# Optimization experiments

Hardware: AMD Instinct MI355X
Metric: run time of the kernel (lower is better)

## Reference

```python
import jax, jax.numpy as jnp
import numpy as np

N_HEADS = 8
EMBED_C = 256  # key/query channels
OUT_C = 256    # value/output channels
MASK_CENTER = True

def setup_inputs() -> dict:
    key = jax.random.key(0)
    ks = jax.random.split(key, 5)
    B, C, H, W = 32, 256, 32, 32
    x = jax.random.normal(ks[0], (B, C, H, W), dtype=jnp.float32)
    # 1x1 conv weights as [out, in] matrices; scaled like torch conv default init
    s = 1.0 / np.sqrt(C)
    q_w = jax.random.normal(ks[1], (EMBED_C, C), dtype=jnp.float32) * s
    q_b = jax.random.normal(ks[2], (EMBED_C,), dtype=jnp.float32) * s
    kv_w = jax.random.normal(ks[3], (EMBED_C + OUT_C, C), dtype=jnp.float32) * s
    kv_b = jax.random.normal(ks[4], (EMBED_C + OUT_C,), dtype=jnp.float32) * s
    return {"x": x, "q_w": q_w, "q_b": q_b, "kv_w": kv_w, "kv_b": kv_b}

def _to_multihead(t):
    # t: (B, C, S) -> (B, n_heads, S, C // n_heads)
    B, C, S = t.shape
    return jnp.transpose(t.reshape(B, N_HEADS, C // N_HEADS, S), (0, 1, 3, 2))

def reference(x, q_w, q_b, kv_w, kv_b):
    B, C, H, W = x.shape
    S = H * W
    xf = x.reshape(B, C, S)  # flatten spatial; 1x1 conv == channel matmul
    q = jnp.einsum('oc,bcs->bos', q_w, xf) + q_b[None, :, None]
    kv = jnp.einsum('oc,bcs->bos', kv_w, xf) + kv_b[None, :, None]
    k, v = kv[:, :EMBED_C], kv[:, EMBED_C:]
    q = _to_multihead(q)   # (B, h, S, dk)
    k = _to_multihead(k)   # (B, h, S, dk)
    v = _to_multihead(v)   # (B, h, S, dv)
    dk = k.shape[-1]
    # strictly-lower-triangular causal mask (center pixel masked)
    mask = jnp.tril(jnp.ones((S, S), dtype=x.dtype), -int(MASK_CENTER))
    scores = jnp.einsum('bhqd,bhkd->bhqk', q, k) / jnp.sqrt(jnp.asarray(dk, x.dtype))
    scores = jnp.where(mask == 0, jnp.asarray(-10000.0, x.dtype), scores)
    attn = jax.nn.softmax(scores, axis=-1)
    attn = jnp.where(mask == 0, jnp.asarray(0.0, x.dtype), attn)
    out = jnp.einsum('bhqk,bhkd->bhqd', attn, v)  # (B, h, S, dv)
    out = jnp.transpose(out, (0, 1, 3, 2)).reshape(B, OUT_C, H, W)
    return out
```

## Files before the change

kernel.cpp:

```cpp
#include <hip/hip_runtime.h>
#include <hip/hip_bf16.h>

typedef __attribute__((ext_vector_type(8))) short short8;
typedef __attribute__((ext_vector_type(4))) float f32x4;
typedef __attribute__((ext_vector_type(16))) float f32x16;

#define B_  32
#define CH  256
#define S_  1024
#define NH  8
#define HD  32

static __device__ __forceinline__ unsigned short f2bf(float f) {
  __hip_bfloat16 h = __float2bfloat16(f);
  return *reinterpret_cast<unsigned short*>(&h);
}

static __device__ __forceinline__ void gl_lds16(const void* g, void* l) {
  __builtin_amdgcn_global_load_lds(
      (const __attribute__((address_space(1))) void*)g,
      (__attribute__((address_space(3))) void*)l, 16, 0, 0);
}

__global__ void k_prep(const float* __restrict__ x, unsigned short* __restrict__ xt,
                       const float* __restrict__ qw, const float* __restrict__ qb,
                       const float* __restrict__ kvw, const float* __restrict__ kvb,
                       unsigned short* __restrict__ wt, float* __restrict__ bias) {
  __shared__ float tile[32][33];
  int blk = (int)blockIdx.x;
  int t = threadIdx.x;
  if (blk < 8192) {
    int b = blk >> 8;
    int inner = blk & 255;
    int ct = inner >> 5, st = inner & 31;
    int c0 = ct * 32, s0 = st * 32;
    int r = t >> 3, q4 = (t & 7) * 4;
    const float4 v = *reinterpret_cast<const float4*>(
        x + ((size_t)(b * CH + c0 + r)) * S_ + s0 + q4);
    tile[r][q4 + 0] = v.x; tile[r][q4 + 1] = v.y;
    tile[r][q4 + 2] = v.z; tile[r][q4 + 3] = v.w;
    __syncthreads();
    ushort4 u;
    u.x = f2bf(tile[q4 + 0][r]); u.y = f2bf(tile[q4 + 1][r]);
    u.z = f2bf(tile[q4 + 2][r]); u.w = f2bf(tile[q4 + 3][r]);
    *reinterpret_cast<ushort4*>(xt + ((size_t)(b * S_ + s0 + r)) * CH + c0 + q4) = u;
  } else {
    int gid = (blk - 8192) * 256 + t;
    const float rs = 0.25503531838951954f;
    int o = gid >> 8, c = gid & 255;
    float v = (o < 256) ? qw[o * 256 + c] * rs : kvw[(o - 256) * 256 + c];
    wt[gid] = f2bf(v);
    if (gid < 768) bias[gid] = (gid < 256) ? qb[gid] * rs : kvb[gid - 256];
  }
}

__global__ __launch_bounds__(256, 6) void k_proj(
    const unsigned short* __restrict__ wt, const float* __restrict__ bias,
    const unsigned short* __restrict__ xt,
    unsigned short* __restrict__ qws, unsigned short* __restrict__ kv) {
  __shared__ __align__(16) union {
    struct { unsigned short As[2][2048]; unsigned short Bs[2][2048]; } g;
    unsigned short vst[8192];
  } SH;
  int b = blockIdx.y;
  int mt = blockIdx.x >> 4, nt = blockIdx.x & 15;
  int tid = threadIdx.x;
  int wid = tid >> 6, l = tid & 63;
  int rb = l >> 4, lr = l & 15;
  int wr = wid >> 1, wc = wid & 1;
  int mb = mt * 64, nb = nt * 64;
  int wm = wr * 32, wn = wc * 32;
  const unsigned short* xb = xt + (size_t)b * S_ * CH;

  int r0 = tid >> 2, k0 = (tid & 3) * 8;
  const unsigned short* wa0 = wt + (size_t)(mb + r0) * CH + k0;
  const unsigned short* xb0 = xb + (size_t)(nb + r0) * CH + k0;
  char* asb = (char*)&SH.g.As[0][0];
  char* bsb = (char*)&SH.g.Bs[0][0];
  int wb = wid * 1024;

  f32x4 acc[2][2];
  #pragma unroll
  for (int mf = 0; mf < 2; ++mf)
    #pragma unroll
    for (int nf = 0; nf < 2; ++nf)
      acc[mf][nf] = (f32x4){0.f, 0.f, 0.f, 0.f};

  gl_lds16(wa0, asb + wb);
  gl_lds16(xb0, bsb + wb);
  __syncthreads();

  #pragma unroll 1
  for (int kk = 0; kk < 8; ++kk) {
    int cur = kk & 1;
    if (kk < 7) {
      int ko = (kk + 1) * 32;
      gl_lds16(wa0 + ko, asb + (cur ^ 1) * 4096 + wb);
      gl_lds16(xb0 + ko, bsb + (cur ^ 1) * 4096 + wb);
    }

    short8 a[2], bfr[2];
    #pragma unroll
    for (int mf = 0; mf < 2; ++mf)
      a[mf] = *reinterpret_cast<const short8*>(
          &SH.g.As[cur][(wm + mf * 16 + lr) * 32 + rb * 8]);
    #pragma unroll
    for (int nf = 0; nf < 2; ++nf)
      bfr[nf] = *reinterpret_cast<const short8*>(
          &SH.g.Bs[cur][(wn + nf * 16 + lr) * 32 + rb * 8]);
    #pragma unroll
    for (int mf = 0; mf < 2; ++mf)
      #pragma unroll
      for (int nf = 0; nf < 2; ++nf)
        acc[mf][nf] = __builtin_amdgcn_mfma_f32_16x16x32_bf16(
            a[mf], bfr[nf], acc[mf][nf], 0, 0, 0);

    __syncthreads();
  }

  if (mb < 256) {
    #pragma unroll
    for (int mf = 0; mf < 2; ++mf) {
      int m0 = mb + wm + mf * 16 + rb * 4;
      const float4 bv = *reinterpret_cast<const float4*>(bias + m0);
      #pragma unroll
      for (int nf = 0; nf < 2; ++nf) {
        int n = nb + wn + nf * 16 + lr;
        ushort4 u = {f2bf(acc[mf][nf][0] + bv.x), f2bf(acc[mf][nf][1] + bv.y),
                     f2bf(acc[mf][nf][2] + bv.z), f2bf(acc[mf][nf][3] + bv.w)};
        int h = m0 >> 5, d = m0 & 31;
        *reinterpret_cast<ushort4*>(
            qws + ((size_t)(b * NH + h) * S_ + n) * HD + d) = u;
      }
    }
  } else {
    const bool isV = (mb >= 512);
    const int voff = isV ? 1024 : 0;
    unsigned short* vst = SH.vst;
    #pragma unroll
    for (int mf = 0; mf < 2; ++mf) {
      int m0 = mb + wm + mf * 16 + rb * 4;
      const float4 bv = *reinterpret_cast<const float4*>(bias + m0);
      int mml = wm + mf * 16 + rb * 4;
      int hl = mml >> 5, d0 = mml & 31;
      #pragma unroll
      for (int nf = 0; nf < 2; ++nf) {
        int nlc = wn + nf * 16 + lr;
        int tl = nlc >> 5, nl = nlc & 31;
        float v0 = acc[mf][nf][0] + bv.x;
        float v1 = acc[mf][nf][1] + bv.y;
        float v2 = acc[mf][nf][2] + bv.z;
        float v3 = acc[mf][nf][3] + bv.w;
        int tb = (hl * 2 + tl) * 1024;
        if (isV) {
          int kp = (nl & 19) | (((nl >> 2) & 1) << 3) | (((nl >> 3) & 1) << 2);
          int base = tb + (kp >> 3) * 256 + (kp & 7);
          vst[base + (size_t)(d0 + 0) * 8] = f2bf(v0);
          vst[base + (size_t)(d0 + 1) * 8] = f2bf(v1);
          vst[base + (size_t)(d0 + 2) * 8] = f2bf(v2);
          vst[base + (size_t)(d0 + 3) * 8] = f2bf(v3);
        } else {
          ushort4 u = {f2bf(v0), f2bf(v1), f2bf(v2), f2bf(v3)};
          *reinterpret_cast<ushort4*>(
              &vst[tb + (d0 >> 3) * 256 + nl * 8 + (d0 & 7)]) = u;
        }
      }
    }
    __syncthreads();
    int tt = tid >> 6, j = tid & 63;
    int hb = (isV ? (mb - 512) : (mb - 256)) >> 5;
    int h = hb + (tt >> 1);
    size_t gb = ((size_t)(b * NH + h) * 32 + (nt * 2 + (tt & 1))) * 2048 + voff;
    #pragma unroll
    for (int s = 0; s < 2; ++s) {
      int off = (j + s * 64) * 8;
      *reinterpret_cast<short8*>(kv + gb + off) =
          *reinterpret_cast<const short8*>(vst + tt * 1024 + off);
    }
  }
}

__global__ __launch_bounds__(512, 4) void k_attn(
    const unsigned short* __restrict__ qws, const unsigned short* __restrict__ kv,
    float* __restrict__ out) {
  __shared__ __align__(16) unsigned short kvbuf[2][8192];
  int tid = threadIdx.x;
  int wid = tid >> 6, l = tid & 63;
  int col = l & 31, hi = l >> 5;
  int bh = (int)(blockIdx.x & 255);
  int g  = 3 - (int)(blockIdx.x >> 8);
  int qt = g * 8 + wid;
  int q0 = qt << 5;
  int niter = g * 2 + 2;

  const unsigned short* Q   = qws + (size_t)bh * S_ * HD;
  const unsigned short* kvb = kv + (size_t)bh * 32 * 2048;
  char* kb0 = (char*)&kvbuf[0][0];
  int wb = wid * 1024;

  short8 aq0 = *reinterpret_cast<const short8*>(Q + (q0 + col) * HD + hi * 8);
  short8 aq1 = *reinterpret_cast<const short8*>(Q + (q0 + col) * HD + 16 + hi * 8);

  f32x16 z, O;
  #pragma unroll
  for (int i = 0; i < 16; ++i) { z[i] = 0.f; O[i] = 0.f; }
  float lsA = 0.f, lsB = 0.f;

  gl_lds16(kvb + tid * 8,        kb0 + wb);
  gl_lds16(kvb + 4096 + tid * 8, kb0 + 8192 + wb);
  __syncthreads();

  #pragma unroll 1
  for (int i = 0; i < niter; ++i) {
    int cur = i & 1;
    bool more = (i + 1 < niter);
    if (more) {
      const unsigned short* src = kvb + (size_t)(i + 1) * 8192 + tid * 8;
      char* dst = kb0 + (cur ^ 1) * 16384 + wb;
      gl_lds16(src,        dst);
      gl_lds16(src + 4096, dst + 8192);
    }

    #pragma unroll
    for (int sub = 0; sub < 4; ++sub) {
      int t = 4 * i + sub;
      if (qt >= t) {
        const unsigned short* Kb = &kvbuf[cur][sub * 2048];
        short8 bk0 = *reinterpret_cast<const short8*>(Kb + hi * 256 + col * 8);
        short8 bk1 = *reinterpret_cast<const short8*>(Kb + 512 + hi * 256 + col * 8);
        short8 av0 = *reinterpret_cast<const short8*>(Kb + 1024 + hi * 256 + col * 8);
        short8 av1 = *reinterpret_cast<const short8*>(Kb + 1536 + hi * 256 + col * 8);

        f32x16 st = __builtin_amdgcn_mfma_f32_32x32x16_bf16(bk0, aq0, z, 0, 0, 0);
        st = __builtin_amdgcn_mfma_f32_32x32x16_bf16(bk1, aq1, st, 0, 0, 0);

        float p[16];
        if (t == qt) {
          #pragma unroll
          for (int r = 0; r < 16; ++r) {
            int key = (r & 3) + 8 * (r >> 2) + 4 * hi;
            float e = __builtin_amdgcn_exp2f(st[r]);
            p[r] = (key < col) ? e : 0.f;
          }
        } else {
          #pragma unroll
          for (int r = 0; r < 16; ++r) p[r] = __builtin_amdgcn_exp2f(st[r]);
        }

        lsA += ((p[0] + p[1]) + (p[2] + p[3])) + ((p[4] + p[5]) + (p[6] + p[7]));
        lsB += ((p[8] + p[9]) + (p[10] + p[11])) + ((p[12] + p[13]) + (p[14] + p[15]));

        union { unsigned int u[8]; short8 v[2]; } pb;
        #pragma unroll
        for (int jj = 0; jj < 8; ++jj)
          asm("v_cvt_pk_bf16_f32 %0, %1, %2"
              : "=v"(pb.u[jj]) : "v"(p[2 * jj]), "v"(p[2 * jj + 1]));

        O = __builtin_amdgcn_mfma_f32_32x32x16_bf16(av0, pb.v[0], O, 0, 0, 0);
        O = __builtin_amdgcn_mfma_f32_32x32x16_bf16(av1, pb.v[1], O, 0, 0, 0);
      }
    }

    __syncthreads();
  }

  float lsum = lsA + lsB;
  float ltot = lsum + __shfl_xor(lsum, 32);
  float linv = (ltot > 0.f) ? 1.f / ltot : 0.f;
  int b = bh >> 3, h = bh & 7;
  float* ob = out + ((size_t)(b * 256 + h * 32)) * S_ + q0 + col;
  #pragma unroll
  for (int r = 0; r < 16; ++r) {
    int d = (r & 3) + 8 * (r >> 2) + 4 * hi;
    ob[(size_t)d * S_] = O[r] * linv;
  }
}

extern "C" void kernel_launch(void* const* d_in, const int* in_sizes, int n_in,
                              void* d_out, int out_size, void* d_ws, size_t ws_size,
                              hipStream_t stream) {
  const float* x   = (const float*)d_in[0];
  const float* qw  = (const float*)d_in[1];
  const float* qb  = (const float*)d_in[2];
  const float* kvw = (const float*)d_in[3];
  const float* kvb = (const float*)d_in[4];
  float* out = (float*)d_out;

  char* ws = (char*)d_ws;
  unsigned short* wt   = (unsigned short*)(ws + 0);
  float*          bias = (float*)(ws + 393216);
  unsigned short* xt   = (unsigned short*)(ws + 396288);
  unsigned short* qws  = (unsigned short*)(ws + 17173504);
  unsigned short* kv   = (unsigned short*)(ws + 33950720);

  k_prep<<<8960, 256, 0, stream>>>(x, xt, qw, qb, kvw, kvb, wt, bias);
  k_proj<<<dim3(192, 32), 256, 0, stream>>>(wt, bias, xt, qws, kv);
  k_attn<<<1024, 512, 0, stream>>>(qws, kv, out);
}
```

Before: 77.79 us.

## Keep X tile resident in LDS and loop projection over all output rows

The projection kernel now loads each 64-column slice of the transposed input into LDS once (full K=256) and has a 512-thread block loop over all 768 output channels in 128-row chunks. Weight fragments are read directly from global memory into registers with a small software prefetch, instead of being staged through double-buffered LDS. This removes re-reading the same X tile for each of the 12 output-row tiles and drops per-k-step barriers. The trade-off is a much smaller grid (512 blocks), serialized output-row work per block, and uncached global weight loads on the MFMA critical path.

Result: no change. 76.87 us (-1.2%).

```diff
diff --git a/kernel.cpp b/kernel.cpp
--- a/kernel.cpp
+++ b/kernel.cpp
@@ -54,128 +54,118 @@
   }
 }
 
-__global__ __launch_bounds__(256, 6) void k_proj(
+__global__ __launch_bounds__(512) void k_proj(
     const unsigned short* __restrict__ wt, const float* __restrict__ bias,
     const unsigned short* __restrict__ xt,
     unsigned short* __restrict__ qws, unsigned short* __restrict__ kv) {
-  __shared__ __align__(16) union {
-    struct { unsigned short As[2][2048]; unsigned short Bs[2][2048]; } g;
-    unsigned short vst[8192];
-  } SH;
-  int b = blockIdx.y;
-  int mt = blockIdx.x >> 4, nt = blockIdx.x & 15;
+  __shared__ __align__(16) unsigned short Bs[16384];
+  __shared__ __align__(16) unsigned short vst[8192];
+  int b = (int)blockIdx.x >> 4, nt = (int)blockIdx.x & 15;
   int tid = threadIdx.x;
   int wid = tid >> 6, l = tid & 63;
   int rb = l >> 4, lr = l & 15;
-  int wr = wid >> 1, wc = wid & 1;
-  int mb = mt * 64, nb = nt * 64;
-  int wm = wr * 32, wn = wc * 32;
+  int nb = nt * 64;
   const unsigned short* xb = xt + (size_t)b * S_ * CH;
 
-  int r0 = tid >> 2, k0 = (tid & 3) * 8;
-  const unsigned short* wa0 = wt + (size_t)(mb + r0) * CH + k0;
-  const unsigned short* xb0 = xb + (size_t)(nb + r0) * CH + k0;
-  char* asb = (char*)&SH.g.As[0][0];
-  char* bsb = (char*)&SH.g.Bs[0][0];
-  int wb = wid * 1024;
-
-  f32x4 acc[2][2];
-  #pragma unroll
-  for (int mf = 0; mf < 2; ++mf)
+  {
+    int row = (tid & 255) >> 2, kkh = tid >> 8, ch = tid & 3;
+    const unsigned short* bsrc = xb + (size_t)(nb + row) * CH + kkh * 32 + ch * 8;
+    char* bsb = (char*)Bs;
+    int wb = wid * 1024;
     #pragma unroll
-    for (int nf = 0; nf < 2; ++nf)
-      acc[mf][nf] = (f32x4){0.f, 0.f, 0.f, 0.f};
-
-  gl_lds16(wa0, asb + wb);
-  gl_lds16(xb0, bsb + wb);
+    for (int q = 0; q < 4; ++q)
+      gl_lds16(bsrc + q * 64, bsb + q * 8192 + wb);
+  }
   __syncthreads();
 
   #pragma unroll 1
-  for (int kk = 0; kk < 8; ++kk) {
-    int cur = kk & 1;
-    if (kk < 7) {
-      int ko = (kk + 1) * 32;
-      gl_lds16(wa0 + ko, asb + (cur ^ 1) * 4096 + wb);
-      gl_lds16(xb0 + ko, bsb + (cur ^ 1) * 4096 + wb);
-    }
-
-    short8 a[2], bfr[2];
+  for (int mt = 0; mt < 6; ++mt) {
+    int mb = mt * 128;
+    const unsigned short* wA = wt + (size_t)(mb + wid * 16 + lr) * CH + rb * 8;
+
+    f32x4 acc[4];
     #pragma unroll
-    for (int mf = 0; mf < 2; ++mf)
-      a[mf] = *reinterpret_cast<const short8*>(
-          &SH.g.As[cur][(wm + mf * 16 + lr) * 32 + rb * 8]);
-    #pragma unroll
-    for (int nf = 0; nf < 2; ++nf)
-      bfr[nf] = *reinterpret_cast<const short8*>(
-          &SH.g.Bs[cur][(wn + nf * 16 + lr) * 32 + rb * 8]);
-    #pragma unroll
-    for (int mf = 0; mf < 2; ++mf)
+    for (int nf = 0; nf < 4; ++nf) acc[nf] = (f32x4){0.f, 0.f, 0.f, 0.f};
+
+#define CMPA(A8, kk) do {                                           \
+    _Pragma("unroll")                                               \
+    for (int nf = 0; nf < 4; ++nf) {                                \
+      short8 bfr = *reinterpret_cast<const short8*>(                \
+          &Bs[(kk) * 2048 + (nf * 16 + lr) * 32 + rb * 8]);         \
+      acc[nf] = __builtin_amdgcn_mfma_f32_16x16x32_bf16(            \
+          A8, bfr, acc[nf], 0, 0, 0);                               \
+    }                                                               \
+  } while (0)
+
+    short8 Pa = *reinterpret_cast<const short8*>(wA);
+    short8 Qa = *reinterpret_cast<const short8*>(wA + 32);
+    CMPA(Pa, 0); Pa = *reinterpret_cast<const short8*>(wA + 64);
+    CMPA(Qa, 1); Qa = *reinterpret_cast<const short8*>(wA + 96);
+    CMPA(Pa, 2); Pa = *reinterpret_cast<const short8*>(wA + 128);
+    CMPA(Qa, 3); Qa = *reinterpret_cast<const short8*>(wA + 160);
+    CMPA(Pa, 4); Pa = *reinterpret_cast<const short8*>(wA + 192);
+    CMPA(Qa, 5); Qa = *reinterpret_cast<const short8*>(wA + 224);
+    CMPA(Pa, 6);
+    CMPA(Qa, 7);
+#undef CMPA
+
+    if (mb < 256) {
+      int m0 = mb + wid * 16 + rb * 4;
+      const float4 bv = *reinterpret_cast<const float4*>(bias + m0);
+      int h = m0 >> 5, d = m0 & 31;
       #pragma unroll
-      for (int nf = 0; nf < 2; ++nf)
-        acc[mf][nf] = __builtin_amdgcn_mfma_f32_16x16x32_bf16(
-            a[mf], bfr[nf], acc[mf][nf], 0, 0, 0);
-
-    __syncthreads();
-  }
-
-  if (mb < 256) {
-    #pragma unroll
-    for (int mf = 0; mf < 2; ++mf) {
-      int m0 = mb + wm + mf * 16 + rb * 4;
-      const float4 bv = *reinterpret_cast<const float4*>(bias + m0);
-      #pragma unroll
-      for (int nf = 0; nf < 2; ++nf) {
-        int n = nb + wn + nf * 16 + lr;
-        ushort4 u = {f2bf(acc[mf][nf][0] + bv.x), f2bf(acc[mf][nf][1] + bv.y),
-                     f2bf(acc[mf][nf][2] + bv.z), f2bf(acc[mf][nf][3] + bv.w)};
-        int h = m0 >> 5, d = m0 & 31;
+      for (int nf = 0; nf < 4; ++nf) {
+        int n = nb + nf * 16 + lr;
+        ushort4 u = {f2bf(acc[nf][0] + bv.x), f2bf(acc[nf][1] + bv.y),
+                     f2bf(acc[nf][2] + bv.z), f2bf(acc[nf][3] + bv.w)};
         *reinterpret_cast<ushort4*>(
             qws + ((size_t)(b * NH + h) * S_ + n) * HD + d) = u;
       }
-    }
-  } else {
-    const bool isV = (mb >= 512);
-    const int voff = isV ? 1024 : 0;
-    unsigned short* vst = SH.vst;
-    #pragma unroll
-    for (int mf = 0; mf < 2; ++mf) {
-      int m0 = mb + wm + mf * 16 + rb * 4;
-      const float4 bv = *reinterpret_cast<const float4*>(bias + m0);
-      int mml = wm + mf * 16 + rb * 4;
-      int hl = mml >> 5, d0 = mml & 31;
-      #pragma unroll
-      for (int nf = 0; nf < 2; ++nf) {
-        int nlc = wn + nf * 16 + lr;
-        int tl = nlc >> 5, nl = nlc & 31;
-        float v0 = acc[mf][nf][0] + bv.x;
-        float v1 = acc[mf][nf][1] + bv.y;
-        float v2 = acc[mf][nf][2] + bv.z;
-        float v3 = acc[mf][nf][3] + bv.w;
-        int tb = (hl * 2 + tl) * 1024;
-        if (isV) {
-          int kp = (nl & 19) | (((nl >> 2) & 1) << 3) | (((nl >> 3) & 1) << 2);
-          int base = tb + (kp >> 3) * 256 + (kp & 7);
-          vst[base + (size_t)(d0 + 0) * 8] = f2bf(v0);
-          vst[base + (size_t)(d0 + 1) * 8] = f2bf(v1);
-          vst[base + (size_t)(d0 + 2) * 8] = f2bf(v2);
-          vst[base + (size_t)(d0 + 3) * 8] = f2bf(v3);
-        } else {
-          ushort4 u = {f2bf(v0), f2bf(v1), f2bf(v2), f2bf(v3)};
-          *reinterpret_cast<ushort4*>(
-              &vst[tb + (d0 >> 3) * 256 + nl * 8 + (d0 & 7)]) = u;
+    } else {
+      const bool isV = (mb >= 512);
+      const int voff = isV ? 1024 : 0;
+      __syncthreads();
+      {
+        int m0 = mb + wid * 16 + rb * 4;
+        const float4 bv = *reinterpret_cast<const float4*>(bias + m0);
+        int mml = wid * 16 + rb * 4;
+        int hl = mml >> 5, d0 = mml & 31;
+        #pragma unroll
+        for (int nf = 0; nf < 4; ++nf) {
+          int nlc = nf * 16 + lr;
+          int tl = nlc >> 5, nl = nlc & 31;
+          float v0 = acc[nf][0] + bv.x;
+          float v1 = acc[nf][1] + bv.y;
+          float v2 = acc[nf][2] + bv.z;
+          float v3 = acc[nf][3] + bv.w;
+          int tb = (hl * 2 + tl) * 1024;
+          if (isV) {
+            int kp = (nl & 19) | (((nl >> 2) & 1) << 3) | (((nl >> 3) & 1) << 2);
+            int base = tb + (kp >> 3) * 256 + (kp & 7);
+            vst[base + (size_t)(d0 + 0) * 8] = f2bf(v0);
+            vst[base + (size_t)(d0 + 1) * 8] = f2bf(v1);
+            vst[base + (size_t)(d0 + 2) * 8] = f2bf(v2);
+            vst[base + (size_t)(d0 + 3) * 8] = f2bf(v3);
+          } else {
+            ushort4 u = {f2bf(v0), f2bf(v1), f2bf(v2), f2bf(v3)};
+            *reinterpret_cast<ushort4*>(
+                &vst[tb + (d0 >> 3) * 256 + nl * 8 + (d0 & 7)]) = u;
+          }
         }
       }
-    }
-    __syncthreads();
-    int tt = tid >> 6, j = tid & 63;
-    int hb = (isV ? (mb - 512) : (mb - 256)) >> 5;
-    int h = hb + (tt >> 1);
-    size_t gb = ((size_t)(b * NH + h) * 32 + (nt * 2 + (tt & 1))) * 2048 + voff;
-    #pragma unroll
-    for (int s = 0; s < 2; ++s) {
-      int off = (j + s * 64) * 8;
-      *reinterpret_cast<short8*>(kv + gb + off) =
-          *reinterpret_cast<const short8*>(vst + tt * 1024 + off);
+      __syncthreads();
+      {
+        int tt = tid >> 6, j = tid & 63;
+        int hb = (isV ? (mb - 512) : (mb - 256)) >> 5;
+        int h = hb + (tt >> 1);
+        size_t gb = ((size_t)(b * NH + h) * 32 + (nt * 2 + (tt & 1))) * 2048 + voff;
+        #pragma unroll
+        for (int s = 0; s < 2; ++s) {
+          int off = (j + s * 64) * 8;
+          *reinterpret_cast<short8*>(kv + gb + off) =
+              *reinterpret_cast<const short8*>(vst + tt * 1024 + off);
+        }
+      }
     }
   }
 }
@@ -294,6 +284,6 @@
   unsigned short* kv   = (unsigned short*)(ws + 33950720);
 
   k_prep<<<8960, 256, 0, stream>>>(x, xt, qw, qb, kvw, kvb, wt, bias);
-  k_proj<<<dim3(192, 32), 256, 0, stream>>>(wt, bias, xt, qws, kv);
+  k_proj<<<512, 512, 0, stream>>>(wt, bias, xt, qws, kv);
   k_attn<<<1024, 512, 0, stream>>>(qws, kv, out);
 }
```
